# Kernel tuning notes

Hardware: AMD Instinct MI355X
Metric: run time of the kernel (lower is better)

## Reference

```python
import jax, jax.numpy as jnp
import numpy as np

N_NODES = 50000
N_EDGES = 800000
NODE_F = 64
HID = 64
LSTM_F = 32
LSTM_H = 128
B = 64
T = 200
OUT = 1
N_LAYERS = 2


def setup_inputs() -> dict:
    key = jax.random.key(0)
    ks = jax.random.split(key, 16)
    s = 0.05
    return {
        "x": jax.random.normal(ks[0], (N_NODES, NODE_F), jnp.float32),
        "edge_attr": jax.random.normal(ks[1], (N_EDGES, NODE_F), jnp.float32),
        "x_seq": jax.random.normal(ks[2], (B, T, LSTM_F), jnp.float32),
        "lin_W": jax.random.normal(ks[3], (N_LAYERS, HID, HID), jnp.float32) * s,
        "lin_b": jnp.zeros((N_LAYERS, HID), jnp.float32),
        "mlp_W1": jax.random.normal(ks[4], (N_LAYERS, HID, HID), jnp.float32) * s,
        "mlp_b1": jnp.zeros((N_LAYERS, HID), jnp.float32),
        "mlp_W2": jax.random.normal(ks[5], (N_LAYERS, HID, HID), jnp.float32) * s,
        "mlp_b2": jnp.zeros((N_LAYERS, HID), jnp.float32),
        "eps": jnp.zeros((N_LAYERS,), jnp.float32),
        "ln_scale": jnp.ones((N_LAYERS, HID), jnp.float32),
        "ln_bias": jnp.zeros((N_LAYERS, HID), jnp.float32),
        "W_ih": jax.random.normal(ks[6], (4 * LSTM_H, HID + LSTM_F), jnp.float32) * s,
        "W_hh": jax.random.normal(ks[7], (4 * LSTM_H, LSTM_H), jnp.float32) * s,
        "b_ih": jnp.zeros((4 * LSTM_H,), jnp.float32),
        "b_hh": jnp.zeros((4 * LSTM_H,), jnp.float32),
        "lstm_ln_scale": jnp.ones((LSTM_H,), jnp.float32),
        "lstm_ln_bias": jnp.zeros((LSTM_H,), jnp.float32),
        "fc_W": jax.random.normal(ks[8], (OUT, LSTM_H), jnp.float32) * s,
        "fc_b": jnp.zeros((OUT,), jnp.float32),
        "edge_index": jax.random.randint(ks[9], (2, N_EDGES), 0, N_NODES, jnp.int32),
        "node_indices": jax.random.randint(ks[10], (B,), 0, N_NODES, jnp.int32),
    }


def _layernorm(z, scale, bias, eps=1e-5):
    mu = jnp.mean(z, axis=-1, keepdims=True)
    var = jnp.var(z, axis=-1, keepdims=True)
    return (z - mu) * jax.lax.rsqrt(var + eps) * scale + bias


def reference(x, edge_attr, x_seq, lin_W, lin_b, mlp_W1, mlp_b1, mlp_W2, mlp_b2,
              eps, ln_scale, ln_bias, W_ih, W_hh, b_ih, b_hh,
              lstm_ln_scale, lstm_ln_bias, fc_W, fc_b, edge_index, node_indices):
    src, dst = edge_index[0], edge_index[1]
    h = x
    n = x.shape[0]
    # GINEConv layers: out = MLP((1+eps)*x + sum_j relu(x_j + lin(e_ij)))
    for l in range(N_LAYERS):
        e = edge_attr @ lin_W[l].T + lin_b[l]            # [E, C]
        m = jax.nn.relu(h[src] + e)                       # gather + message
        agg = jax.ops.segment_sum(m, dst, num_segments=n) # scatter-add
        z = (1.0 + eps[l]) * h + agg
        z = jax.nn.relu(z @ mlp_W1[l].T + mlp_b1[l]) @ mlp_W2[l].T + mlp_b2[l]
        z = _layernorm(z, ln_scale[l], ln_bias[l])
        h = jax.nn.relu(z)

    sel = h[node_indices]                                 # [B, HID]
    seq_len = x_seq.shape[1]
    expanded = jnp.broadcast_to(sel[:, None, :], (sel.shape[0], seq_len, sel.shape[1]))
    combined = jnp.concatenate([expanded, x_seq], axis=2) # [B, T, HID+F]

    # single-layer LSTM, PyTorch gate order (i, f, g, o)
    Hd = W_hh.shape[1]
    xs = jnp.transpose(combined, (1, 0, 2))               # [T, B, D]
    x_proj = xs @ W_ih.T + b_ih                            # [T, B, 4H]

    def step(carry, xp):
        hprev, cprev = carry
        gates = xp + hprev @ W_hh.T + b_hh
        i, f, g, o = jnp.split(gates, 4, axis=-1)
        i = jax.nn.sigmoid(i); f = jax.nn.sigmoid(f)
        g = jnp.tanh(g); o = jax.nn.sigmoid(o)
        c = f * cprev + i * g
        hn = o * jnp.tanh(c)
        return (hn, c), None

    bsz = combined.shape[0]
    init = (jnp.zeros((bsz, Hd), combined.dtype), jnp.zeros((bsz, Hd), combined.dtype))
    (hn, _), _ = jax.lax.scan(step, init, x_proj)

    last = _layernorm(hn, lstm_ln_scale, lstm_ln_bias)
    return last @ fc_W.T + fc_b
```

## Files before the change

### kernel.cpp

```cpp
#include <hip/hip_runtime.h>
#include <cmath>

static constexpr int NN  = 50000;
static constexpr int NE  = 800000;
static constexpr int HID = 64;
static constexpr int BB  = 64;
static constexpr int TT  = 200;
static constexpr int LH  = 128;
static constexpr int G4  = 512;
static constexpr int NTILES = NE / 64;

static constexpr int SCB = 125;
static constexpr int SCH = 400;

typedef _Float16 h2 __attribute__((ext_vector_type(2)));
typedef _Float16 h8 __attribute__((ext_vector_type(8)));
typedef float    f4 __attribute__((ext_vector_type(4)));

#ifndef __has_builtin
#define __has_builtin(x) 0
#endif
#if __has_builtin(__builtin_amdgcn_fdot2)
__device__ __forceinline__ float fdot2_(h2 a, h2 b, float c) {
    return __builtin_amdgcn_fdot2(a, b, c, false);
}
#else
__device__ __forceinline__ float fdot2_(h2 a, h2 b, float c) {
    return c + (float)a.x * (float)b.x + (float)a.y * (float)b.y;
}
#endif

__device__ __forceinline__ h2 as_h2(unsigned int u) {
    union { unsigned int u; h2 h; } cv; cv.u = u; return cv.h;
}

__device__ __forceinline__ float sigmoid_fast(float x) {
    return __fdividef(1.f, 1.f + __expf(-x));
}
__device__ __forceinline__ float tanh_fast(float x) {
    return __fdividef(2.f, 1.f + __expf(-2.f * x)) - 1.f;
}

__global__ __launch_bounds__(256) void hist_kernel(const int* __restrict__ dsts,
                                                   int* __restrict__ deg) {
    int i = blockIdx.x * 256 + threadIdx.x;
    if (i < NE) atomicAdd(&deg[dsts[i]], 1);
}

__global__ __launch_bounds__(512) void scan1_kernel(const int* __restrict__ deg,
                                                    int* __restrict__ loc,
                                                    int* __restrict__ bsum) {
    __shared__ int ws[8];
    const int b = blockIdx.x, t = threadIdx.x;
    const int idx = b * SCH + t;
    const int lane = t & 63, wv = t >> 6;
    int v = (t < SCH && idx < NN) ? deg[idx] : 0;
    int x = v;
    #pragma unroll
    for (int off = 1; off < 64; off <<= 1) {
        int y = __shfl_up(x, off);
        if (lane >= off) x += y;
    }
    if (lane == 63) ws[wv] = x;
    __syncthreads();
    if (t < 8) {
        int s = ws[t];
        #pragma unroll
        for (int off = 1; off < 8; off <<= 1) {
            int y = __shfl_up(s, off);
            if (t >= off) s += y;
        }
        ws[t] = s;
    }
    __syncthreads();
    const int base = wv ? ws[wv - 1] : 0;
    if (t < SCH && idx < NN) loc[idx] = base + x - v;
    if (t == 511) bsum[b] = ws[7];
}

__global__ void scan2_kernel(const int* __restrict__ bsum,
                             int* __restrict__ boff,
                             int* __restrict__ rowptr) {
    int tot = 0;
    for (int i = 0; i < SCB; ++i) { boff[i] = tot; tot += bsum[i]; }
    rowptr[NN] = tot;
}

__global__ __launch_bounds__(512) void scan3_kernel(const int* __restrict__ loc,
                                                    const int* __restrict__ boff,
                                                    int* __restrict__ rowptr,
                                                    int* __restrict__ head) {
    const int b = blockIdx.x, t = threadIdx.x;
    const int idx = b * SCH + t;
    if (t < SCH && idx < NN) {
        int r = loc[idx] + boff[b];
        rowptr[idx] = r;
        head[idx] = r;
    }
}

__global__ __launch_bounds__(256) void scatter_kernel(const int* __restrict__ srcs,
                                                      const int* __restrict__ dsts,
                                                      int* __restrict__ head,
                                                      int* __restrict__ perm,
                                                      int* __restrict__ ssrc,
                                                      int* __restrict__ sdst) {
    int e = blockIdx.x * 256 + threadIdx.x;
    if (e < NE) {
        int d = dsts[e];
        int pos = atomicAdd(&head[d], 1);
        perm[e] = pos;
        ssrc[pos] = srcs[e];
        sdst[pos] = d;
    }
}

__global__ __launch_bounds__(256) void permute_kernel(const float* __restrict__ ea,
                                                      const int* __restrict__ perm,
                                                      ushort4* __restrict__ easort) {
    const int lane = threadIdx.x & 63, wid = threadIdx.x >> 6;
    const int slot = lane >> 4, hw = lane & 15;
    const int e = (blockIdx.x * 4 + wid) * 4 + slot;
    if (e < NE) {
        const int p = perm[e];
        float4 v = ((const float4*)ea)[(size_t)e * 16 + hw];
        union { _Float16 h[4]; ushort4 u; } pk;
        pk.h[0] = (_Float16)v.x; pk.h[1] = (_Float16)v.y;
        pk.h[2] = (_Float16)v.z; pk.h[3] = (_Float16)v.w;
        easort[(size_t)p * 16 + hw] = pk.u;
    }
}

__global__ __launch_bounds__(256) void cvt16_kernel(const float* __restrict__ in,
                                                    _Float16* __restrict__ o) {
    int i = blockIdx.x * 256 + threadIdx.x;
    float4 v = ((const float4*)in)[i];
    union { _Float16 h[4]; ushort4 u; } pk;
    pk.h[0] = (_Float16)v.x; pk.h[1] = (_Float16)v.y;
    pk.h[2] = (_Float16)v.z; pk.h[3] = (_Float16)v.w;
    ((ushort4*)o)[i] = pk.u;
}

__global__ __launch_bounds__(256) void edge_mfma_kernel(
    const _Float16* __restrict__ h16,
    const _Float16* __restrict__ easort,
    const float*    __restrict__ W,
    const float*    __restrict__ bias,
    const int*      __restrict__ ssrc,
    const int*      __restrict__ sdst,
    float*          __restrict__ agg)
{
    __shared__ _Float16 atile[64 * 64];
    __shared__ _Float16 etile[64 * 64];
    const int t    = threadIdx.x;
    const int lane = t & 63;
    const int w    = t >> 6;
    const int c15  = lane & 15;
    const int g    = lane >> 4;

    h8 bfr[4][2];
    #pragma unroll
    for (int ct = 0; ct < 4; ++ct) {
        #pragma unroll
        for (int ks = 0; ks < 2; ++ks) {
            const float* wp = W + (size_t)(ct * 16 + c15) * 64 + ks * 32 + g * 8;
            float4 f0 = ((const float4*)wp)[0];
            float4 f1 = ((const float4*)wp)[1];
            h8 b;
            b[0] = (_Float16)f0.x; b[1] = (_Float16)f0.y;
            b[2] = (_Float16)f0.z; b[3] = (_Float16)f0.w;
            b[4] = (_Float16)f1.x; b[5] = (_Float16)f1.y;
            b[6] = (_Float16)f1.z; b[7] = (_Float16)f1.w;
            bfr[ct][ks] = b;
        }
    }
    float bi[4];
    #pragma unroll
    for (int ct = 0; ct < 4; ++ct) bi[ct] = bias[ct * 16 + c15];

    const int u0 = t, u1 = t + 256;
    const int row0 = u0 >> 3, off0 = (u0 & 7) * 16;
    const int row1 = u1 >> 3, off1 = (u1 & 7) * 16;
    uint4* const at0 = (uint4*)((char*)atile + row0 * 128 + (off0 ^ ((row0 & 7) << 4)));
    uint4* const at1 = (uint4*)((char*)atile + row1 * 128 + (off1 ^ ((row1 & 7) << 4)));

    int tile = blockIdx.x;
    {
        const uint4* src = (const uint4*)(easort + (size_t)tile * 64 * 64);
        *at0 = src[u0];
        *at1 = src[u1];
    }
    __syncthreads();

    while (true) {
        const int next = tile + gridDim.x;

        f4 acc[4];
        #pragma unroll
        for (int ct = 0; ct < 4; ++ct) { acc[ct][0]=0.f; acc[ct][1]=0.f; acc[ct][2]=0.f; acc[ct][3]=0.f; }
        const int arow = w * 16 + c15;
        #pragma unroll
        for (int ks = 0; ks < 2; ++ks) {
            h8 a = *(const h8*)((const char*)atile + arow * 128 +
                                ((ks * 64 + g * 16) ^ ((arow & 7) << 4)));
            #pragma unroll
            for (int ct = 0; ct < 4; ++ct)
                acc[ct] = __builtin_amdgcn_mfma_f32_16x16x32_f16(a, bfr[ct][ks], acc[ct], 0, 0, 0);
        }

        uint4 st0, st1;
        const bool more = (next < NTILES);
        if (more) {
            const uint4* src = (const uint4*)(easort + (size_t)next * 64 * 64);
            st0 = src[u0];
            st1 = src[u1];
        }

        #pragma unroll
        for (int ct = 0; ct < 4; ++ct) {
            #pragma unroll
            for (int r = 0; r < 4; ++r) {
                int slot = w * 16 + g * 4 + r;
                float v = acc[ct][r] + bi[ct];
                *(_Float16*)((char*)etile + slot * 128 +
                             (((ct * 16 + c15) * 2) ^ ((slot & 7) << 4))) = (_Float16)v;
            }
        }

        const int wbase = tile * 64 + w * 16;
        const int sdv = sdst[wbase + (lane & 15)];
        const int ssv = ssrc[wbase + (lane & 15)];
        float hv[16];
        #pragma unroll
        for (int i = 0; i < 16; ++i) {
            int sj = __shfl(ssv, i);
            hv[i] = (float)h16[(size_t)sj * HID + lane];
        }
        asm volatile("s_waitcnt lgkmcnt(0)" ::: "memory");

        int prev = __shfl(sdv, 0);
        float accv = 0.f;
        #pragma unroll
        for (int i = 0; i < 16; ++i) {
            int d = __shfl(sdv, i);
            if (d != prev) {
                unsafeAtomicAdd(&agg[(size_t)prev * HID + lane], accv);
                accv = 0.f; prev = d;
            }
            const int slot = w * 16 + i;
            float ev = (float)*(const _Float16*)((const char*)etile + slot * 128 +
                                                 ((lane * 2) ^ ((slot & 7) << 4)));
            float m = ev + hv[i];
            accv += m > 0.f ? m : 0.f;
        }
        unsafeAtomicAdd(&agg[(size_t)prev * HID + lane], accv);

        if (!more) break;
        __syncthreads();
        *at0 = st0;
        *at1 = st1;
        tile = next;
        __syncthreads();
    }
}

__global__ __launch_bounds__(256) void node_kernel(
    const float* __restrict__ h_in,
    const float* __restrict__ agg,
    const float* __restrict__ W1, const float* __restrict__ b1,
    const float* __restrict__ W2, const float* __restrict__ b2,
    const float* __restrict__ epsp,
    const float* __restrict__ lnS, const float* __restrict__ lnB,
    float*       __restrict__ h_out,
    _Float16*    __restrict__ h16_out)
{
    __shared__ _Float16 zbuf[4][64];
    __shared__ _Float16 tbuf[4][64];
    const int lane = threadIdx.x & 63;
    const int wid  = threadIdx.x >> 6;

    h2 w1h[32], w2h[32];
    {
        const float4* wf1 = (const float4*)(W1 + lane * 64);
        const float4* wf2 = (const float4*)(W2 + lane * 64);
        #pragma unroll
        for (int k4 = 0; k4 < 16; ++k4) {
            float4 a = wf1[k4], b = wf2[k4];
            h2 pa; pa.x = (_Float16)a.x; pa.y = (_Float16)a.y;
            h2 pb; pb.x = (_Float16)a.z; pb.y = (_Float16)a.w;
            w1h[2*k4] = pa; w1h[2*k4+1] = pb;
            h2 pc; pc.x = (_Float16)b.x; pc.y = (_Float16)b.y;
            h2 pd; pd.x = (_Float16)b.z; pd.y = (_Float16)b.w;
            w2h[2*k4] = pc; w2h[2*k4+1] = pd;
        }
    }
    const float b1c = b1[lane], b2c = b2[lane];
    const float sC = lnS[lane], bC = lnB[lane];
    const float epv = 1.f + epsp[0];

    const int gw = blockIdx.x * 4 + wid;
    const int nw = gridDim.x * 4;
    for (int n = gw; n < NN; n += nw) {
        float z = epv * h_in[(size_t)n*HID + lane] + agg[(size_t)n*HID + lane];
        zbuf[wid][lane] = (_Float16)z;
        asm volatile("s_waitcnt lgkmcnt(0)" ::: "memory");
        float acc = b1c;
        {
            const uint4* zf = (const uint4*)&zbuf[wid][0];
            #pragma unroll
            for (int k = 0; k < 8; ++k) {
                uint4 u = zf[k];
                acc = fdot2_(as_h2(u.x), w1h[4*k+0], acc);
                acc = fdot2_(as_h2(u.y), w1h[4*k+1], acc);
                acc = fdot2_(as_h2(u.z), w1h[4*k+2], acc);
                acc = fdot2_(as_h2(u.w), w1h[4*k+3], acc);
            }
        }
        acc = acc > 0.f ? acc : 0.f;
        tbuf[wid][lane] = (_Float16)acc;
        asm volatile("s_waitcnt lgkmcnt(0)" ::: "memory");
        float acc2 = b2c;
        {
            const uint4* tf = (const uint4*)&tbuf[wid][0];
            #pragma unroll
            for (int k = 0; k < 8; ++k) {
                uint4 u = tf[k];
                acc2 = fdot2_(as_h2(u.x), w2h[4*k+0], acc2);
                acc2 = fdot2_(as_h2(u.y), w2h[4*k+1], acc2);
                acc2 = fdot2_(as_h2(u.z), w2h[4*k+2], acc2);
                acc2 = fdot2_(as_h2(u.w), w2h[4*k+3], acc2);
            }
        }
        float s1 = acc2, s2 = acc2 * acc2;
        #pragma unroll
        for (int off = 32; off >= 1; off >>= 1) {
            s1 += __shfl_xor(s1, off);
            s2 += __shfl_xor(s2, off);
        }
        float mu  = s1 * (1.f/64.f);
        float var = s2 * (1.f/64.f) - mu * mu;
        float r   = rsqrtf(var + 1e-5f);
        float o   = (acc2 - mu) * r * sC + bC;
        float ov  = o > 0.f ? o : 0.f;
        h_out[(size_t)n*HID + lane] = ov;
        if (h16_out) h16_out[(size_t)n*HID + lane] = (_Float16)ov;
    }
}

__global__ __launch_bounds__(512) void prep_kernel(
    const float* __restrict__ Wih,
    const float* __restrict__ bih,
    const float* __restrict__ h2v,
    const int*   __restrict__ nidx,
    float*       __restrict__ W2T,
    float*       __restrict__ selp)
{
    const int g  = threadIdx.x;
    const int j_ = g & 127, gt_ = g >> 7;
    const int pos = (j_ << 2) | ((gt_ & 1) << 1) | (gt_ >> 1);
    if (blockIdx.x == BB) {
        #pragma unroll
        for (int k = 0; k < 32; ++k)
            W2T[k * G4 + pos] = Wih[g * 96 + 64 + k];
    } else {
        const int b = blockIdx.x;
        __shared__ float hrow[64];
        if (g < 64) hrow[g] = h2v[(size_t)nidx[b] * HID + g];
        __syncthreads();
        float acc = bih[g];
        #pragma unroll
        for (int k = 0; k < 64; ++k)
            acc = fmaf(hrow[k], Wih[g * 96 + k], acc);
        selp[b * G4 + pos] = acc;
    }
}

__global__ __launch_bounds__(512) void xp_kernel(
    const float* __restrict__ xseq,
    const float* __restrict__ selp,
    const float* __restrict__ W2T,
    float*       __restrict__ xp)
{
    const int g   = threadIdx.x;
    const int row = blockIdx.x;
    const int t   = row >> 6;
    const int b   = row & 63;
    __shared__ float xs[32];
    if (g < 32) xs[g] = xseq[((size_t)b * TT + t) * 32 + g];
    __syncthreads();
    float acc = selp[b * G4 + g];
    #pragma unroll
    for (int k = 0; k < 32; ++k)
        acc = fmaf(xs[k], W2T[k * G4 + g], acc);
    xp[(size_t)row * G4 + g] = acc;
}

__global__ __launch_bounds__(256) void lstm_kernel(
    const float* __restrict__ xp,
    const float* __restrict__ Whh,
    const float* __restrict__ bhh,
    const float* __restrict__ lnS, const float* __restrict__ lnB,
    const float* __restrict__ fcW,
    const float* __restrict__ fcb,
    float*       __restrict__ out)
{
    const int t  = threadIdx.x;
    const int b  = blockIdx.x;
    const int p  = t & 1;
    const int j  = t >> 1;
    const int gate0 = p * LH + j;
    const int gate1 = (p + 2) * LH + j;

    h2 wA[64], wB[64];
    {
        const float4* wf0 = (const float4*)(Whh + (size_t)gate0 * LH);
        const float4* wf1 = (const float4*)(Whh + (size_t)gate1 * LH);
        #pragma unroll
        for (int k4 = 0; k4 < 32; ++k4) {
            float4 v = wf0[k4];
            h2 a; a.x = (_Float16)v.x; a.y = (_Float16)v.y;
            h2 c2; c2.x = (_Float16)v.z; c2.y = (_Float16)v.w;
            wA[2*k4] = a; wA[2*k4+1] = c2;
            float4 u = wf1[k4];
            h2 d; d.x = (_Float16)u.x; d.y = (_Float16)u.y;
            h2 e2; e2.x = (_Float16)u.z; e2.y = (_Float16)u.w;
            wB[2*k4] = d; wB[2*k4+1] = e2;
        }
    }
    const float bg0 = bhh[gate0];
    const float bg1 = bhh[gate1];
    const float s1_ = (p == 0) ? 2.f : 1.f;
    const float a1_ = (p == 0) ? 2.f : 1.f;
    const float d1_ = (p == 0) ? -1.f : 0.f;

    __shared__ _Float16 hb[2][LH];
    __shared__ float h_final[LH];
    if (t < 64) ((unsigned int*)&hb[0][0])[t] = 0u;
    float c = 0.f;
    float h_last = 0.f;
    __syncthreads();

    float2 xv = ((const float2*)(xp + (size_t)b * G4))[t];

    auto step = [&](const _Float16* hbR, _Float16* hbW, int ts) {
        const int tn = (ts + 1 < TT) ? ts + 1 : ts;
        const float2 xn = ((const float2*)(xp + ((size_t)tn * BB + b) * G4))[t];

        float a0 = 0.f, a1 = 0.f, a2 = 0.f, a3 = 0.f;
        float e0 = 0.f, e1 = 0.f, e2 = 0.f, e3 = 0.f;
        const uint4* hb4 = (const uint4*)hbR;
        #pragma unroll
        for (int k = 0; k < 16; ++k) {
            uint4 u = hb4[k];
            h2 p0 = as_h2(u.x), p1 = as_h2(u.y), p2 = as_h2(u.z), p3 = as_h2(u.w);
            a0 = fdot2_(p0, wA[4*k+0], a0);
            a1 = fdot2_(p1, wA[4*k+1], a1);
            a2 = fdot2_(p2, wA[4*k+2], a2);
            a3 = fdot2_(p3, wA[4*k+3], a3);
            e0 = fdot2_(p0, wB[4*k+0], e0);
            e1 = fdot2_(p1, wB[4*k+1], e1);
            e2 = fdot2_(p2, wB[4*k+2], e2);
            e3 = fdot2_(p3, wB[4*k+3], e3);
        }
        float g0 = xv.x + bg0 + ((a0 + a1) + (a2 + a3));
        float g1 = xv.y + bg1 + ((e0 + e1) + (e2 + e3));

        float act0 = sigmoid_fast(g0);
        float act1 = fmaf(a1_, __fdividef(1.f, 1.f + __expf(-s1_ * g1)), d1_);

        float o0 = __shfl_xor(act0, 1);
        float o1 = __shfl_xor(act1, 1);
        float iv = p ? o0 : act0;
        float fv = p ? act0 : o0;
        float gv = p ? o1 : act1;
        float ov = p ? act1 : o1;

        c = fmaf(fv, c, iv * gv);
        h_last = ov * tanh_fast(c);

        if (p == 0) hbW[j] = (_Float16)h_last;
        __syncthreads();

        xv = xn;
    };

    for (int ts = 0; ts < TT; ts += 2) {
        step(&hb[0][0], &hb[1][0], ts);
        step(&hb[1][0], &hb[0][0], ts + 1);
    }

    if (p == 0) h_final[j] = h_last;
    __syncthreads();
    if (t < 64) {
        float h0 = h_final[t], h1 = h_final[t + 64];
        float s1 = h0 + h1, s2 = h0*h0 + h1*h1;
        #pragma unroll
        for (int off = 32; off >= 1; off >>= 1) {
            s1 += __shfl_xor(s1, off);
            s2 += __shfl_xor(s2, off);
        }
        float mu  = s1 * (1.f/128.f);
        float var = s2 * (1.f/128.f) - mu * mu;
        float rr  = rsqrtf(var + 1e-5f);
        float pv = ((h0 - mu)*rr*lnS[t]      + lnB[t])      * fcW[t]
                 + ((h1 - mu)*rr*lnS[t + 64] + lnB[t + 64]) * fcW[t + 64];
        #pragma unroll
        for (int off = 32; off >= 1; off >>= 1) pv += __shfl_xor(pv, off);
        if (t == 0) out[b] = pv + fcb[0];
    }
}

extern "C" void kernel_launch(void* const* d_in, const int* in_sizes, int n_in,
                              void* d_out, int out_size, void* d_ws, size_t ws_size,
                              hipStream_t stream) {
    const float* x     = (const float*)d_in[0];
    const float* ea    = (const float*)d_in[1];
    const float* xseq  = (const float*)d_in[2];
    const float* linW  = (const float*)d_in[3];
    const float* linB  = (const float*)d_in[4];
    const float* mW1   = (const float*)d_in[5];
    const float* mb1   = (const float*)d_in[6];
    const float* mW2   = (const float*)d_in[7];
    const float* mb2   = (const float*)d_in[8];
    const float* eps   = (const float*)d_in[9];
    const float* lnS   = (const float*)d_in[10];
    const float* lnB   = (const float*)d_in[11];
    const float* Wih   = (const float*)d_in[12];
    const float* Whh   = (const float*)d_in[13];
    const float* bih   = (const float*)d_in[14];
    const float* bhh   = (const float*)d_in[15];
    const float* llnS  = (const float*)d_in[16];
    const float* llnB  = (const float*)d_in[17];
    const float* fcW   = (const float*)d_in[18];
    const float* fcb   = (const float*)d_in[19];
    const int*   eidx  = (const int*)d_in[20];
    const int*   nidx  = (const int*)d_in[21];
    float* out = (float*)d_out;

    const int* srcs = eidx;
    const int* dsts = eidx + NE;

    float* ws   = (float*)d_ws;
    float* agg  = ws;
    float* h1   = agg  + (size_t)NN * HID;
    float* h2m  = h1   + (size_t)NN * HID;
    float* selp = h2m  + (size_t)NN * HID;
    float* W2T  = selp + (size_t)BB * G4;
    float* xp   = W2T  + (size_t)32 * G4;
    int*   deg    = (int*)(xp + (size_t)TT * BB * G4);
    int*   rowptr = deg + NN;
    int*   head   = rowptr + NN + 2;
    int*   loc    = head + NN;
    int*   bsum   = loc + NN;
    int*   boff   = bsum + SCB + 3;
    int*   perm   = boff + SCB + 3;
    int*   ssrc   = perm + NE;
    int*   sdst   = ssrc + NE;
    uintptr_t ep = (uintptr_t)(sdst + NE);
    ep = (ep + 15) & ~(uintptr_t)15;
    _Float16* easort = (_Float16*)ep;
    _Float16* x16    = easort + (size_t)NE * HID;
    _Float16* h1_16  = x16 + (size_t)NN * HID;

    const size_t aggBytes = (size_t)NN * HID * sizeof(float);

    hipMemsetAsync(deg, 0, (size_t)NN * sizeof(int), stream);
    hist_kernel<<<(NE + 255) / 256, 256, 0, stream>>>(dsts, deg);
    scan1_kernel<<<SCB, 512, 0, stream>>>(deg, loc, bsum);
    scan2_kernel<<<1, 1, 0, stream>>>(bsum, boff, rowptr);
    scan3_kernel<<<SCB, 512, 0, stream>>>(loc, boff, rowptr, head);
    scatter_kernel<<<(NE + 255) / 256, 256, 0, stream>>>(srcs, dsts, head, perm, ssrc, sdst);
    permute_kernel<<<NE / 16, 256, 0, stream>>>(ea, perm, (ushort4*)easort);
    cvt16_kernel<<<NN * HID / 4 / 256, 256, 0, stream>>>(x, x16);

    hipMemsetAsync(agg, 0, aggBytes, stream);
    edge_mfma_kernel<<<2048, 256, 0, stream>>>(x16, easort, linW, linB, ssrc, sdst, agg);
    node_kernel<<<512, 256, 0, stream>>>(x, agg, mW1, mb1, mW2, mb2, eps, lnS, lnB, h1, h1_16);
    hipMemsetAsync(agg, 0, aggBytes, stream);
    edge_mfma_kernel<<<2048, 256, 0, stream>>>(h1_16, easort, linW + 64*64, linB + 64, ssrc, sdst, agg);
    node_kernel<<<512, 256, 0, stream>>>(h1, agg, mW1 + 64*64, mb1 + 64, mW2 + 64*64, mb2 + 64,
                                         eps + 1, lnS + 64, lnB + 64, h2m, (_Float16*)nullptr);
    prep_kernel<<<BB + 1, 512, 0, stream>>>(Wih, bih, h2m, nidx, W2T, selp);
    xp_kernel<<<TT * BB, 512, 0, stream>>>(xseq, selp, W2T, xp);
    lstm_kernel<<<BB, 256, 0, stream>>>(xp, Whh, bhh, llnS, llnB, fcW, fcb, out);
}
```

Baseline: 558.2 us.

## Batch LSTM recurrence over 16 sequences per block using MFMA f16 tiles

The LSTM recurrence previously ran one block per sequence, doing the h·W_hh product with fdot2 instructions. It now runs on 4 blocks, each handling 16 batch rows. The hidden-state matmul uses mfma_f32_16x16x32_f16, with W_hh fragments held in registers and h kept in swizzled LDS. The xp kernel writes its output in a blocked layout that matches the MFMA accumulator layout, so each lane can prefetch its gate inputs with vector loads. The intent is to cut the per-step cost of the sequential recurrence, at the cost of more activation work per lane and only 4 CUs in use.

```diff
diff --git a/kernel.cpp b/kernel.cpp
--- a/kernel.cpp
+++ b/kernel.cpp
@@ -355,13 +355,11 @@
     float*       __restrict__ W2T,
     float*       __restrict__ selp)
 {
-    const int g  = threadIdx.x;
-    const int j_ = g & 127, gt_ = g >> 7;
-    const int pos = (j_ << 2) | ((gt_ & 1) << 1) | (gt_ >> 1);
+    const int g = threadIdx.x;
     if (blockIdx.x == BB) {
         #pragma unroll
         for (int k = 0; k < 32; ++k)
-            W2T[k * G4 + pos] = Wih[g * 96 + 64 + k];
+            W2T[k * G4 + g] = Wih[g * 96 + 64 + k];
     } else {
         const int b = blockIdx.x;
         __shared__ float hrow[64];
@@ -371,7 +369,7 @@
         #pragma unroll
         for (int k = 0; k < 64; ++k)
             acc = fmaf(hrow[k], Wih[g * 96 + k], acc);
-        selp[b * G4 + pos] = acc;
+        selp[b * G4 + g] = acc;
     }
 }
 
@@ -379,24 +377,32 @@
     const float* __restrict__ xseq,
     const float* __restrict__ selp,
     const float* __restrict__ W2T,
-    float*       __restrict__ xp)
+    float*       __restrict__ xpb)
 {
-    const int g   = threadIdx.x;
+    const int G   = threadIdx.x;
     const int row = blockIdx.x;
     const int t   = row >> 6;
     const int b   = row & 63;
     __shared__ float xs[32];
-    if (g < 32) xs[g] = xseq[((size_t)b * TT + t) * 32 + g];
+    if (G < 32) xs[G] = xseq[((size_t)b * TT + t) * 32 + G];
     __syncthreads();
-    float acc = selp[b * G4 + g];
+    float acc = selp[b * G4 + G];
     #pragma unroll
     for (int k = 0; k < 32; ++k)
-        acc = fmaf(xs[k], W2T[k * G4 + g], acc);
-    xp[(size_t)row * G4 + g] = acc;
-}
-
-__global__ __launch_bounds__(256) void lstm_kernel(
-    const float* __restrict__ xp,
+        acc = fmaf(xs[k], W2T[k * G4 + G], acc);
+
+    const int blk = b >> 4, col = b & 15;
+    const int T  = G >> 7, j = G & 127;
+    const int uidx = j >> 4, w = uidx >> 1, q = uidx & 1;
+    const int ti = T * 2 + q;
+    const int g4 = (j >> 2) & 3, r = j & 3;
+    const int lane = g4 * 16 + col;
+    const size_t idx = (size_t)t * 32768 + blk * 8192 + w * 2048 + ti * 256 + lane * 4 + r;
+    xpb[idx] = acc;
+}
+
+__global__ __launch_bounds__(256) void lstm_mfma_kernel(
+    const float* __restrict__ xpb,
     const float* __restrict__ Whh,
     const float* __restrict__ bhh,
     const float* __restrict__ lnS, const float* __restrict__ lnB,
@@ -404,109 +410,137 @@
     const float* __restrict__ fcb,
     float*       __restrict__ out)
 {
-    const int t  = threadIdx.x;
-    const int b  = blockIdx.x;
-    const int p  = t & 1;
-    const int j  = t >> 1;
-    const int gate0 = p * LH + j;
-    const int gate1 = (p + 2) * LH + j;
-
-    h2 wA[64], wB[64];
+    const int tid  = threadIdx.x;
+    const int blk  = blockIdx.x;
+    const int w    = tid >> 6;
+    const int lane = tid & 63;
+    const int c15  = lane & 15;
+    const int g    = lane >> 4;
+
+    h8 afr[8][4];
+    float bb[8][4];
+    #pragma unroll
+    for (int ti = 0; ti < 8; ++ti) {
+        const int m = (ti >> 1) * 8 + w * 2 + (ti & 1);
+        #pragma unroll
+        for (int ks = 0; ks < 4; ++ks) {
+            const float* wp = Whh + (size_t)(m * 16 + c15) * LH + ks * 32 + g * 8;
+            float4 f0 = ((const float4*)wp)[0];
+            float4 f1 = ((const float4*)wp)[1];
+            h8 a;
+            a[0] = (_Float16)f0.x; a[1] = (_Float16)f0.y;
+            a[2] = (_Float16)f0.z; a[3] = (_Float16)f0.w;
+            a[4] = (_Float16)f1.x; a[5] = (_Float16)f1.y;
+            a[6] = (_Float16)f1.z; a[7] = (_Float16)f1.w;
+            afr[ti][ks] = a;
+        }
+        #pragma unroll
+        for (int r = 0; r < 4; ++r)
+            bb[ti][r] = bhh[m * 16 + g * 4 + r];
+    }
+
+    __shared__ _Float16 Hs[2][16 * 128];
+    ((uint4*)&Hs[0][0])[tid] = make_uint4(0, 0, 0, 0);
+    float cst[2][4];
+    #pragma unroll
+    for (int q = 0; q < 2; ++q)
+        #pragma unroll
+        for (int r = 0; r < 4; ++r) cst[q][r] = 0.f;
+    __syncthreads();
+
+    const float* xbase = xpb + (size_t)blk * 8192 + w * 2048 + lane * 4;
+    f4 cur[8];
+    #pragma unroll
+    for (int ti = 0; ti < 8; ++ti)
+        cur[ti] = *(const f4*)(xbase + ti * 256);
+
+    const int wq0 = (w * 2 + 0) * 32 + g * 8;
+    const int wq1 = (w * 2 + 1) * 32 + g * 8;
+
+    for (int t = 0; t < TT; ++t) {
+        const int rd = t & 1, wr = rd ^ 1;
+        const char* hsr = (const char*)&Hs[rd][0] + c15 * 256;
+        char* hsw = (char*)&Hs[wr][0] + c15 * 256;
+
+        h8 bfr[4];
+        #pragma unroll
+        for (int ks = 0; ks < 4; ++ks)
+            bfr[ks] = *(const h8*)(hsr + ((ks * 64 + g * 16) ^ ((c15 & 7) << 4)));
+
+        f4 nxt[8];
+        if (t + 1 < TT) {
+            const float* xb = xbase + (size_t)(t + 1) * 32768;
+            #pragma unroll
+            for (int ti = 0; ti < 8; ++ti)
+                nxt[ti] = *(const f4*)(xb + ti * 256);
+        }
+
+        f4 acc[8];
+        #pragma unroll
+        for (int ti = 0; ti < 8; ++ti) { acc[ti][0]=0.f; acc[ti][1]=0.f; acc[ti][2]=0.f; acc[ti][3]=0.f; }
+        #pragma unroll
+        for (int ks = 0; ks < 4; ++ks)
+            #pragma unroll
+            for (int ti = 0; ti < 8; ++ti)
+                acc[ti] = __builtin_amdgcn_mfma_f32_16x16x32_f16(afr[ti][ks], bfr[ks], acc[ti], 0, 0, 0);
+
+        union { _Float16 h[4]; uint2 u; } hq0, hq1;
+        #pragma unroll
+        for (int q = 0; q < 2; ++q) {
+            #pragma unroll
+            for (int r = 0; r < 4; ++r) {
+                float gi = acc[0 + q][r] + bb[0 + q][r] + cur[0 + q][r];
+                float gf = acc[2 + q][r] + bb[2 + q][r] + cur[2 + q][r];
+                float gg = acc[4 + q][r] + bb[4 + q][r] + cur[4 + q][r];
+                float go = acc[6 + q][r] + bb[6 + q][r] + cur[6 + q][r];
+                float iv = sigmoid_fast(gi);
+                float fv = sigmoid_fast(gf);
+                float gv = tanh_fast(gg);
+                float ov = sigmoid_fast(go);
+                float cv = fmaf(fv, cst[q][r], iv * gv);
+                cst[q][r] = cv;
+                float hv = ov * tanh_fast(cv);
+                if (q == 0) hq0.h[r] = (_Float16)hv; else hq1.h[r] = (_Float16)hv;
+            }
+        }
+
+        *(uint2*)(hsw + (wq0 ^ ((c15 & 7) << 4))) = hq0.u;
+        *(uint2*)(hsw + (wq1 ^ ((c15 & 7) << 4))) = hq1.u;
+        __syncthreads();
+
+        #pragma unroll
+        for (int ti = 0; ti < 8; ++ti) cur[ti] = nxt[ti];
+    }
+
+    const _Float16* Hf = &Hs[0][0];
     {
-        const float4* wf0 = (const float4*)(Whh + (size_t)gate0 * LH);
-        const float4* wf1 = (const float4*)(Whh + (size_t)gate1 * LH);
-        #pragma unroll
-        for (int k4 = 0; k4 < 32; ++k4) {
-            float4 v = wf0[k4];
-            h2 a; a.x = (_Float16)v.x; a.y = (_Float16)v.y;
-            h2 c2; c2.x = (_Float16)v.z; c2.y = (_Float16)v.w;
-            wA[2*k4] = a; wA[2*k4+1] = c2;
-            float4 u = wf1[k4];
-            h2 d; d.x = (_Float16)u.x; d.y = (_Float16)u.y;
-            h2 e2; e2.x = (_Float16)u.z; e2.y = (_Float16)u.w;
-            wB[2*k4] = d; wB[2*k4+1] = e2;
-        }
-    }
-    const float bg0 = bhh[gate0];
-    const float bg1 = bhh[gate1];
-    const float s1_ = (p == 0) ? 2.f : 1.f;
-    const float a1_ = (p == 0) ? 2.f : 1.f;
-    const float d1_ = (p == 0) ? -1.f : 0.f;
-
-    __shared__ _Float16 hb[2][LH];
-    __shared__ float h_final[LH];
-    if (t < 64) ((unsigned int*)&hb[0][0])[t] = 0u;
-    float c = 0.f;
-    float h_last = 0.f;
-    __syncthreads();
-
-    float2 xv = ((const float2*)(xp + (size_t)b * G4))[t];
-
-    auto step = [&](const _Float16* hbR, _Float16* hbW, int ts) {
-        const int tn = (ts + 1 < TT) ? ts + 1 : ts;
-        const float2 xn = ((const float2*)(xp + ((size_t)tn * BB + b) * G4))[t];
-
-        float a0 = 0.f, a1 = 0.f, a2 = 0.f, a3 = 0.f;
-        float e0 = 0.f, e1 = 0.f, e2 = 0.f, e3 = 0.f;
-        const uint4* hb4 = (const uint4*)hbR;
-        #pragma unroll
-        for (int k = 0; k < 16; ++k) {
-            uint4 u = hb4[k];
-            h2 p0 = as_h2(u.x), p1 = as_h2(u.y), p2 = as_h2(u.z), p3 = as_h2(u.w);
-            a0 = fdot2_(p0, wA[4*k+0], a0);
-            a1 = fdot2_(p1, wA[4*k+1], a1);
-            a2 = fdot2_(p2, wA[4*k+2], a2);
-            a3 = fdot2_(p3, wA[4*k+3], a3);
-            e0 = fdot2_(p0, wB[4*k+0], e0);
-            e1 = fdot2_(p1, wB[4*k+1], e1);
-            e2 = fdot2_(p2, wB[4*k+2], e2);
-            e3 = fdot2_(p3, wB[4*k+3], e3);
-        }
-        float g0 = xv.x + bg0 + ((a0 + a1) + (a2 + a3));
-        float g1 = xv.y + bg1 + ((e0 + e1) + (e2 + e3));
-
-        float act0 = sigmoid_fast(g0);
-        float act1 = fmaf(a1_, __fdividef(1.f, 1.f + __expf(-s1_ * g1)), d1_);
-
-        float o0 = __shfl_xor(act0, 1);
-        float o1 = __shfl_xor(act1, 1);
-        float iv = p ? o0 : act0;
-        float fv = p ? act0 : o0;
-        float gv = p ? o1 : act1;
-        float ov = p ? act1 : o1;
-
-        c = fmaf(fv, c, iv * gv);
-        h_last = ov * tanh_fast(c);
-
-        if (p == 0) hbW[j] = (_Float16)h_last;
-        __syncthreads();
-
-        xv = xn;
-    };
-
-    for (int ts = 0; ts < TT; ts += 2) {
-        step(&hb[0][0], &hb[1][0], ts);
-        step(&hb[1][0], &hb[0][0], ts + 1);
-    }
-
-    if (p == 0) h_final[j] = h_last;
-    __syncthreads();
-    if (t < 64) {
-        float h0 = h_final[t], h1 = h_final[t + 64];
-        float s1 = h0 + h1, s2 = h0*h0 + h1*h1;
-        #pragma unroll
-        for (int off = 32; off >= 1; off >>= 1) {
+        const int col = tid >> 4, kk = tid & 15;
+        h8 hvv = *(const h8*)((const char*)Hf + col * 256 + ((kk * 16) ^ ((col & 7) << 4)));
+        float hh[8];
+        float s1 = 0.f, s2 = 0.f;
+        #pragma unroll
+        for (int i = 0; i < 8; ++i) {
+            hh[i] = (float)hvv[i];
+            s1 += hh[i];
+            s2 += hh[i] * hh[i];
+        }
+        #pragma unroll
+        for (int off = 8; off >= 1; off >>= 1) {
             s1 += __shfl_xor(s1, off);
             s2 += __shfl_xor(s2, off);
         }
-        float mu  = s1 * (1.f/128.f);
-        float var = s2 * (1.f/128.f) - mu * mu;
+        float mu  = s1 * (1.f / 128.f);
+        float var = s2 * (1.f / 128.f) - mu * mu;
         float rr  = rsqrtf(var + 1e-5f);
-        float pv = ((h0 - mu)*rr*lnS[t]      + lnB[t])      * fcW[t]
-                 + ((h1 - mu)*rr*lnS[t + 64] + lnB[t + 64]) * fcW[t + 64];
-        #pragma unroll
-        for (int off = 32; off >= 1; off >>= 1) pv += __shfl_xor(pv, off);
-        if (t == 0) out[b] = pv + fcb[0];
+        float p = 0.f;
+        #pragma unroll
+        for (int i = 0; i < 8; ++i) {
+            int k = kk * 8 + i;
+            p += ((hh[i] - mu) * rr * lnS[k] + lnB[k]) * fcW[k];
+        }
+        #pragma unroll
+        for (int off = 8; off >= 1; off >>= 1) p += __shfl_xor(p, off);
+        if (kk == 0) out[blk * 16 + col] = p + fcb[0];
     }
 }
 
@@ -546,8 +580,8 @@
     float* h2m  = h1   + (size_t)NN * HID;
     float* selp = h2m  + (size_t)NN * HID;
     float* W2T  = selp + (size_t)BB * G4;
-    float* xp   = W2T  + (size_t)32 * G4;
-    int*   deg    = (int*)(xp + (size_t)TT * BB * G4);
+    float* xpb  = W2T  + (size_t)32 * G4;
+    int*   deg    = (int*)(xpb + (size_t)TT * BB * G4);
     int*   rowptr = deg + NN;
     int*   head   = rowptr + NN + 2;
     int*   loc    = head + NN;
@@ -581,6 +615,6 @@
     node_kernel<<<512, 256, 0, stream>>>(h1, agg, mW1 + 64*64, mb1 + 64, mW2 + 64*64, mb2 + 64,
                                          eps + 1, lnS + 64, lnB + 64, h2m, (_Float16*)nullptr);
     prep_kernel<<<BB + 1, 512, 0, stream>>>(Wih, bih, h2m, nidx, W2T, selp);
-    xp_kernel<<<TT * BB, 512, 0, stream>>>(xseq, selp, W2T, xp);
-    lstm_kernel<<<BB, 256, 0, stream>>>(xp, Whh, bhh, llnS, llnB, fcW, fcb, out);
-}
+    xp_kernel<<<TT * BB, 512, 0, stream>>>(xseq, selp, W2T, xpb);
+    lstm_mfma_kernel<<<4, 256, 0, stream>>>(xpb, Whh, bhh, llnS, llnB, fcW, fcb, out);
+}
```

Result: slower. 833.1 us (+49.2%).
